# Kernel tuning notes

Hardware: AMD Instinct MI355X
Metric: run time of the kernel (lower is better)

## Reference

```python
import jax, jax.numpy as jnp
import numpy as np

H = 2048      # hidden_size
K = 1024      # bottleneck_size
R = 3         # number of roles
B = 8         # batch
S = 2048      # sequence length
LN_EPS = 1e-5


def setup_inputs() -> dict:
    key = jax.random.key(0)
    ks = jax.random.split(key, 8)
    # torch nn.Linear default init ~ U(-1/sqrt(fan_in), 1/sqrt(fan_in)); scale similarly
    sd_d = 1.0 / np.sqrt(H)
    sd_u = 1.0 / np.sqrt(K)
    return {
        "role": jax.random.randint(ks[0], (B,), 0, R),
        "hidden_states": jax.random.normal(ks[1], (B, S, H), dtype=jnp.float32),
        # stacked per-role adapter params
        "W_down": jax.random.uniform(ks[2], (R, H, K), jnp.float32, -sd_d, sd_d),
        "b_down": jax.random.uniform(ks[3], (R, K), jnp.float32, -sd_d, sd_d),
        "W_up": jax.random.uniform(ks[4], (R, K, H), jnp.float32, -sd_u, sd_u),
        "b_up": jax.random.uniform(ks[5], (R, H), jnp.float32, -sd_u, sd_u),
        "gamma": jnp.ones((R, H), jnp.float32),
        "beta": jnp.zeros((R, H), jnp.float32),
    }


def reference(role, hidden_states, W_down, b_down, W_up, b_up, gamma, beta):
    # gather per-sample adapter params by role id: [B, H, K] etc.
    h = jnp.einsum("bsh,bhk->bsk", hidden_states, W_down[role]) + b_down[role][:, None, :]
    h = jax.nn.gelu(h, approximate=False)  # torch nn.GELU default = exact erf
    u = jnp.einsum("bsk,bkh->bsh", h, W_up[role]) + b_up[role][:, None, :]
    y = hidden_states + u
    # LayerNorm over last dim
    mean = jnp.mean(y, axis=-1, keepdims=True)
    var = jnp.mean(jnp.square(y - mean), axis=-1, keepdims=True)
    yn = (y - mean) * jax.lax.rsqrt(var + LN_EPS)
    return yn * gamma[role][:, None, :] + beta[role][:, None, :]
```

## Files before the change

kernel.cpp:

```cpp
#include <hip/hip_runtime.h>
#include <hip/hip_bf16.h>

#define H 2048
#define K 1024
#define R 3
#define BB 8
#define S 2048

typedef __bf16 bf16x8 __attribute__((ext_vector_type(8)));
typedef float f32x4 __attribute__((ext_vector_type(4)));
typedef unsigned short ushort8 __attribute__((ext_vector_type(8)));

static __device__ __forceinline__ unsigned short f2bf(float f) {
    unsigned int u = __float_as_uint(f);
    u += 0x7FFFu + ((u >> 16) & 1u);
    return (unsigned short)(u >> 16);
}

#define GLOAD_LDS16(g, l)                                                      \
    __builtin_amdgcn_global_load_lds(                                          \
        (const __attribute__((address_space(1))) void*)(g),                    \
        (__attribute__((address_space(3))) void*)(l), 16, 0, 0)

__global__ __launch_bounds__(256) void cvt_hs(const float* __restrict__ in,
                                              unsigned short* __restrict__ out,
                                              int n8) {
    int stride = gridDim.x * blockDim.x;
    for (int i = blockIdx.x * blockDim.x + threadIdx.x; i < n8; i += stride) {
        const float4* p = (const float4*)(in + (size_t)i * 8);
        float4 a = p[0], b = p[1];
        union { unsigned short us[8]; ushort8 v; } o;
        o.us[0] = f2bf(a.x); o.us[1] = f2bf(a.y);
        o.us[2] = f2bf(a.z); o.us[3] = f2bf(a.w);
        o.us[4] = f2bf(b.x); o.us[5] = f2bf(b.y);
        o.us[6] = f2bf(b.z); o.us[7] = f2bf(b.w);
        *(ushort8*)(out + (size_t)i * 8) = o.v;
    }
}

__global__ __launch_bounds__(256) void tpose(const float* __restrict__ in,
                                             unsigned short* __restrict__ out,
                                             int rows, int cols) {
    __shared__ float tile[32][33];
    int rr = blockIdx.z;
    const float* ip = in + (size_t)rr * rows * cols;
    unsigned short* op = out + (size_t)rr * rows * cols;
    int x = blockIdx.x * 32 + threadIdx.x;
    int y0 = blockIdx.y * 32 + threadIdx.y;
#pragma unroll
    for (int j = 0; j < 32; j += 8)
        tile[threadIdx.y + j][threadIdx.x] = ip[(size_t)(y0 + j) * cols + x];
    __syncthreads();
    int ox = blockIdx.y * 32 + threadIdx.x;
    int oy0 = blockIdx.x * 32 + threadIdx.y;
#pragma unroll
    for (int j = 0; j < 32; j += 8)
        op[(size_t)(oy0 + j) * rows + ox] = f2bf(tile[threadIdx.x][threadIdx.y + j]);
}

template <int KC, int EPI>
__global__ __launch_bounds__(512, 2) void gemm_8ph(
    const unsigned short* __restrict__ A, const unsigned short* __restrict__ Bt,
    const int* __restrict__ role, const float* __restrict__ bias,
    const unsigned short* __restrict__ resid, void* __restrict__ Out,
    float2* __restrict__ Part, int N) {
    constexpr int NT = KC / 64;
    __shared__ char smem[131072];
    const int tid = threadIdx.x;
    const int wid = tid >> 6, lane = tid & 63;
    const int wm = wid >> 2, wn = wid & 3;
    const int lr = lane & 15, lc = lane >> 4;

    const int nx = N >> 8;
    const int cpx = gridDim.x >> 3;
    const int orig = (blockIdx.x & 7) * cpx + (blockIdx.x >> 3);
    const int tn = orig % nx;
    const int tmz = orig / nx;
    const int tm = tmz & 7;
    const int z = tmz >> 3;
    const int r = role[z];

    const char* Ab = (const char*)(A + ((size_t)z * S + (size_t)tm * 256) * KC);
    const char* Bb = (const char*)(Bt + ((size_t)r * N + (size_t)tn * 256) * KC);

    const int P16 = tid * 16;

#define STAGE16(gbase, ldsoff, kt, half)                                       \
    do {                                                                       \
        _Pragma("unroll") for (int c_ = 0; c_ < 2; c_++) {                     \
            int P_ = c_ * 8192 + P16;                                          \
            int L_ = P_ ^ (((P_ >> 7) & 7) << 4);                              \
            const char* g_ = (gbase) +                                         \
                (size_t)((half) * 128 + (L_ >> 7)) * (KC * 2) +                \
                (size_t)(kt) * 128 + (L_ & 127);                               \
            GLOAD_LDS16(g_, smem + (ldsoff) + (half) * 16384 + P_);            \
        }                                                                      \
    } while (0)

    STAGE16(Ab, 0, 0, 0);        STAGE16(Ab, 0, 0, 1);
    STAGE16(Bb, 32768, 0, 0);    STAGE16(Bb, 32768, 0, 1);
    STAGE16(Bb, 98304, 1, 0);    STAGE16(Bb, 98304, 1, 1);
    asm volatile("s_waitcnt vmcnt(4)" ::: "memory");
    __builtin_amdgcn_s_barrier();

    f32x4 acc[8][4] = {};
    const int swz = (lr & 7) << 4;
    const int ck0 = (lc << 4) ^ swz;
    const int ck1 = ck0 ^ 0x40;
    const char* sm = smem;

#define LDA4(ibase, SL)                                                        \
    _Pragma("unroll") for (int i_ = 0; i_ < 4; i_++) {                         \
        int rb_ = (wm * 128 + ((ibase) + i_) * 16 + lr) << 7;                  \
        a[i_][0] = *(const bf16x8*)(sm + (SL) + rb_ + ck0);                    \
        a[i_][1] = *(const bf16x8*)(sm + (SL) + rb_ + ck1); }
#define LDB2(jbase, SL)                                                        \
    _Pragma("unroll") for (int j_ = 0; j_ < 2; j_++) {                         \
        int rb_ = (wn * 64 + ((jbase) + j_) * 16 + lr) << 7;                   \
        b[(jbase) + j_][0] = *(const bf16x8*)(sm + (SL) + 32768 + rb_ + ck0);  \
        b[(jbase) + j_][1] = *(const bf16x8*)(sm + (SL) + 32768 + rb_ + ck1); }
#define MFMA16(IOFF, JOFF)                                                     \
    _Pragma("unroll") for (int kk = 0; kk < 2; kk++)                           \
    _Pragma("unroll") for (int i_ = 0; i_ < 4; i_++)                           \
    _Pragma("unroll") for (int j_ = 0; j_ < 2; j_++)                           \
        acc[(IOFF) + i_][(JOFF) + j_] = __builtin_amdgcn_mfma_f32_16x16x32_bf16( \
            a[i_][kk], b[(JOFF) + j_][kk], acc[(IOFF) + i_][(JOFF) + j_], 0, 0, 0);
#define PH_MID()                                                               \
    __builtin_amdgcn_s_barrier();                                              \
    asm volatile("s_waitcnt lgkmcnt(0)" ::: "memory");                         \
    __builtin_amdgcn_s_setprio(1);
#define PH_END()                                                               \
    __builtin_amdgcn_s_setprio(0);                                             \
    __builtin_amdgcn_s_barrier();

#pragma unroll 1
    for (int t = 0; t < NT; t += 2) {
        bf16x8 a[4][2], b[4][2];
        const bool pf2 = (t + 2) < NT, pf3 = (t + 3) < NT;
        LDA4(0, 0); LDB2(0, 0);
        STAGE16(Ab, 65536, t + 1, 0);
        asm volatile("s_waitcnt lgkmcnt(8)" ::: "memory");
        PH_MID(); MFMA16(0, 0); PH_END();
        LDB2(2, 0);
        STAGE16(Ab, 65536, t + 1, 1);
        PH_MID(); MFMA16(0, 2); PH_END();
        LDA4(4, 0);
        if (pf2) STAGE16(Bb, 32768, t + 2, 0);
        PH_MID(); MFMA16(4, 0); PH_END();
        if (pf2) STAGE16(Bb, 32768, t + 2, 1);
        PH_MID(); MFMA16(4, 2);
        __builtin_amdgcn_s_setprio(0);
        if (pf2) asm volatile("s_waitcnt vmcnt(4)" ::: "memory");
        else     asm volatile("s_waitcnt vmcnt(0)" ::: "memory");
        __builtin_amdgcn_s_barrier();
        LDA4(0, 65536); LDB2(0, 65536);
        if (pf2) STAGE16(Ab, 0, t + 2, 0);
        asm volatile("s_waitcnt lgkmcnt(8)" ::: "memory");
        PH_MID(); MFMA16(0, 0); PH_END();
        LDB2(2, 65536);
        if (pf2) STAGE16(Ab, 0, t + 2, 1);
        PH_MID(); MFMA16(0, 2); PH_END();
        LDA4(4, 65536);
        if (pf3) STAGE16(Bb, 98304, t + 3, 0);
        PH_MID(); MFMA16(4, 0); PH_END();
        if (pf3) STAGE16(Bb, 98304, t + 3, 1);
        PH_MID(); MFMA16(4, 2);
        __builtin_amdgcn_s_setprio(0);
        if (pf2) {
            if (pf3) asm volatile("s_waitcnt vmcnt(4)" ::: "memory");
            else     asm volatile("s_waitcnt vmcnt(0)" ::: "memory");
            __builtin_amdgcn_s_barrier();
        }
    }
#undef STAGE16
#undef LDA4
#undef LDB2
#undef MFMA16
#undef PH_MID
#undef PH_END

    const int base_m = tm * 256 + wm * 128;
    const int base_n = tn * 256 + wn * 64;
    float bn[4];
    const float* bp = bias + (size_t)r * N + base_n;
#pragma unroll
    for (int j = 0; j < 4; j++) bn[j] = bp[j * 16 + lr];

    if (EPI == 0) {
        unsigned short* o = (unsigned short*)Out;
#pragma unroll
        for (int i = 0; i < 8; i++) {
#pragma unroll
            for (int j = 0; j < 4; j++) {
#pragma unroll
                for (int q = 0; q < 4; q++) {
                    size_t grow = (size_t)z * S + base_m + i * 16 + lc * 4 + q;
                    int col = base_n + j * 16 + lr;
                    float x = acc[i][j][q] + bn[j];
                    float g = 0.5f * x * (1.0f + erff(x * 0.70710678118654752f));
                    o[grow * N + col] = f2bf(g);
                }
            }
        }
    } else {
        unsigned short* o = (unsigned short*)Out;
        float* pl = (float*)smem;
        __syncthreads();
#pragma unroll
        for (int i = 0; i < 8; i++) {
#pragma unroll
            for (int q = 0; q < 4; q++) {
                size_t grow = (size_t)z * S + base_m + i * 16 + lc * 4 + q;
                float s = 0.f, sq = 0.f;
#pragma unroll
                for (int j = 0; j < 4; j++) {
                    int col = base_n + j * 16 + lr;
                    float rv = __uint_as_float(((unsigned)resid[grow * (size_t)N + col]) << 16);
                    float y = acc[i][j][q] + bn[j] + rv;
                    o[grow * (size_t)N + col] = f2bf(y);
                    s += y; sq += y * y;
                }
#pragma unroll
                for (int off = 1; off < 16; off <<= 1) {
                    s  += __shfl_xor(s, off);
                    sq += __shfl_xor(sq, off);
                }
                if (lr == 0) {
                    int rloc = wm * 128 + i * 16 + lc * 4 + q;
                    pl[wn * 256 + rloc] = s;
                    pl[(4 + wn) * 256 + rloc] = sq;
                }
            }
        }
        __syncthreads();
        if (tid < 256) {
            float s  = pl[tid] + pl[256 + tid] + pl[512 + tid] + pl[768 + tid];
            float sq = pl[1024 + tid] + pl[1280 + tid] + pl[1536 + tid] + pl[1792 + tid];
            size_t grow = (size_t)z * S + tm * 256 + tid;
            Part[(size_t)tn * (BB * S) + grow] = make_float2(s, sq);
        }
    }
}

__global__ __launch_bounds__(256) void ln2(const unsigned short* __restrict__ ybf,
                                           const float2* __restrict__ part,
                                           const int* __restrict__ role,
                                           const float* __restrict__ gamma,
                                           const float* __restrict__ beta,
                                           float* __restrict__ out) {
    int row = blockIdx.x;
    int z = row >> 11;
    int r = role[z];
    float s = 0.f, ss = 0.f;
#pragma unroll
    for (int nb = 0; nb < 8; nb++) {
        float2 p = part[(size_t)nb * (BB * S) + row];
        s += p.x; ss += p.y;
    }
    float mean = s * (1.0f / H);
    float var = ss * (1.0f / H) - mean * mean;
    float rstd = rsqrtf(var + 1e-5f);
    int t = threadIdx.x;
    ushort8 yv = ((const ushort8*)(ybf + (size_t)row * H))[t];
    const float4* gp = (const float4*)(gamma + (size_t)r * H);
    const float4* bp = (const float4*)(beta + (size_t)r * H);
    float4 g0 = gp[2 * t], g1 = gp[2 * t + 1];
    float4 b0 = bp[2 * t], b1 = bp[2 * t + 1];
    float yo[8];
#pragma unroll
    for (int e = 0; e < 8; e++)
        yo[e] = (__uint_as_float(((unsigned)yv[e]) << 16) - mean) * rstd;
    float4 r0, r1;
    r0.x = yo[0] * g0.x + b0.x; r0.y = yo[1] * g0.y + b0.y;
    r0.z = yo[2] * g0.z + b0.z; r0.w = yo[3] * g0.w + b0.w;
    r1.x = yo[4] * g1.x + b1.x; r1.y = yo[5] * g1.y + b1.y;
    r1.z = yo[6] * g1.z + b1.z; r1.w = yo[7] * g1.w + b1.w;
    float4* op = (float4*)(out + (size_t)row * H);
    op[2 * t] = r0;
    op[2 * t + 1] = r1;
}

extern "C" void kernel_launch(void* const* d_in, const int* in_sizes, int n_in,
                              void* d_out, int out_size, void* d_ws, size_t ws_size,
                              hipStream_t stream) {
    const int* role = (const int*)d_in[0];
    const float* hs = (const float*)d_in[1];
    const float* Wd = (const float*)d_in[2];
    const float* bd = (const float*)d_in[3];
    const float* Wu = (const float*)d_in[4];
    const float* bu = (const float*)d_in[5];
    const float* gamma = (const float*)d_in[6];
    const float* beta = (const float*)d_in[7];
    float* out = (float*)d_out;

    char* ws = (char*)d_ws;
    unsigned short* hs_bf = (unsigned short*)ws;
    unsigned short* y_bf = (unsigned short*)ws;
    unsigned short* wd_t = (unsigned short*)(ws + 67108864);
    float2* part = (float2*)(ws + 67108864);
    unsigned short* wu_t = (unsigned short*)(ws + 67108864 + 12582912);
    unsigned short* h_ws = (unsigned short*)(ws + 67108864 + 2 * 12582912);

    cvt_hs<<<4096, 256, 0, stream>>>(hs, hs_bf, (BB * S * H) / 8);
    dim3 tb(32, 8);
    tpose<<<dim3(K / 32, H / 32, R), tb, 0, stream>>>(Wd, wd_t, H, K);
    tpose<<<dim3(H / 32, K / 32, R), tb, 0, stream>>>(Wu, wu_t, K, H);
    gemm_8ph<H, 0><<<(K / 256) * 8 * BB, 512, 0, stream>>>(hs_bf, wd_t, role, bd,
                                                           nullptr, h_ws, nullptr, K);
    gemm_8ph<K, 1><<<(H / 256) * 8 * BB, 512, 0, stream>>>(h_ws, wu_t, role, bu,
                                                           hs_bf, y_bf, part, H);
    ln2<<<BB * S, 256, 0, stream>>>(y_bf, part, role, gamma, beta, out);
}
```

Baseline: 256.0 us.

## Software-pipeline LDS fragment reads one phase ahead of MFMA in GEMM loop

Restructures the GEMM main loop so LDS fragment reads for the next quadrant are issued before the MFMAs of the current quadrant. A and B fragments are double-buffered in registers (aA/aB, bL/bH), and the per-phase barrier/lgkmcnt(0) pairs are replaced with a single barrier per phase. The first tile's fragments are read in a prologue. The intent is to hide LDS latency behind matrix work and cut barrier count. This costs more VGPRs, and the relaxed vmcnt and barrier placement risks races on the staged buffers.

```diff
diff --git a/kernel.cpp b/kernel.cpp
--- a/kernel.cpp
+++ b/kernel.cpp
@@ -101,7 +101,7 @@
     STAGE16(Bb, 32768, 0, 0);    STAGE16(Bb, 32768, 0, 1);
     STAGE16(Bb, 98304, 1, 0);    STAGE16(Bb, 98304, 1, 1);
     asm volatile("s_waitcnt vmcnt(4)" ::: "memory");
-    __builtin_amdgcn_s_barrier();
+    asm volatile("s_barrier" ::: "memory");
 
     f32x4 acc[8][4] = {};
     const int swz = (lr & 7) << 4;
@@ -109,75 +109,75 @@
     const int ck1 = ck0 ^ 0x40;
     const char* sm = smem;
 
-#define LDA4(ibase, SL)                                                        \
+    bf16x8 aA[4][2], aB[4][2], bL[2][2], bH[2][2];
+
+#define RDA(dst, ibase, SL)                                                    \
     _Pragma("unroll") for (int i_ = 0; i_ < 4; i_++) {                         \
         int rb_ = (wm * 128 + ((ibase) + i_) * 16 + lr) << 7;                  \
-        a[i_][0] = *(const bf16x8*)(sm + (SL) + rb_ + ck0);                    \
-        a[i_][1] = *(const bf16x8*)(sm + (SL) + rb_ + ck1); }
-#define LDB2(jbase, SL)                                                        \
+        dst[i_][0] = *(const bf16x8*)(sm + (SL) + rb_ + ck0);                  \
+        dst[i_][1] = *(const bf16x8*)(sm + (SL) + rb_ + ck1); }
+#define RDB(dst, jbase, SL)                                                    \
     _Pragma("unroll") for (int j_ = 0; j_ < 2; j_++) {                         \
         int rb_ = (wn * 64 + ((jbase) + j_) * 16 + lr) << 7;                   \
-        b[(jbase) + j_][0] = *(const bf16x8*)(sm + (SL) + 32768 + rb_ + ck0);  \
-        b[(jbase) + j_][1] = *(const bf16x8*)(sm + (SL) + 32768 + rb_ + ck1); }
-#define MFMA16(IOFF, JOFF)                                                     \
+        dst[j_][0] = *(const bf16x8*)(sm + (SL) + 32768 + rb_ + ck0);          \
+        dst[j_][1] = *(const bf16x8*)(sm + (SL) + 32768 + rb_ + ck1); }
+#define QMFMA(ar, br, IOFF, JOFF)                                              \
     _Pragma("unroll") for (int kk = 0; kk < 2; kk++)                           \
     _Pragma("unroll") for (int i_ = 0; i_ < 4; i_++)                           \
     _Pragma("unroll") for (int j_ = 0; j_ < 2; j_++)                           \
         acc[(IOFF) + i_][(JOFF) + j_] = __builtin_amdgcn_mfma_f32_16x16x32_bf16( \
-            a[i_][kk], b[(JOFF) + j_][kk], acc[(IOFF) + i_][(JOFF) + j_], 0, 0, 0);
-#define PH_MID()                                                               \
-    __builtin_amdgcn_s_barrier();                                              \
-    asm volatile("s_waitcnt lgkmcnt(0)" ::: "memory");                         \
-    __builtin_amdgcn_s_setprio(1);
-#define PH_END()                                                               \
-    __builtin_amdgcn_s_setprio(0);                                             \
-    __builtin_amdgcn_s_barrier();
+            ar[i_][kk], br[j_][kk], acc[(IOFF) + i_][(JOFF) + j_], 0, 0, 0);
+#define BAR() asm volatile("s_barrier" ::: "memory")
+
+    RDA(aA, 0, 0);
+    RDB(bL, 0, 0);
 
 #pragma unroll 1
     for (int t = 0; t < NT; t += 2) {
-        bf16x8 a[4][2], b[4][2];
-        const bool pf2 = (t + 2) < NT, pf3 = (t + 3) < NT;
-        LDA4(0, 0); LDB2(0, 0);
+        const bool pf = (t + 2) < NT;
+        RDB(bH, 2, 0);
         STAGE16(Ab, 65536, t + 1, 0);
-        asm volatile("s_waitcnt lgkmcnt(8)" ::: "memory");
-        PH_MID(); MFMA16(0, 0); PH_END();
-        LDB2(2, 0);
+        __builtin_amdgcn_s_setprio(1); QMFMA(aA, bL, 0, 0);
+        __builtin_amdgcn_s_setprio(0); BAR();
+        RDA(aB, 4, 0);
         STAGE16(Ab, 65536, t + 1, 1);
-        PH_MID(); MFMA16(0, 2); PH_END();
-        LDA4(4, 0);
-        if (pf2) STAGE16(Bb, 32768, t + 2, 0);
-        PH_MID(); MFMA16(4, 0); PH_END();
-        if (pf2) STAGE16(Bb, 32768, t + 2, 1);
-        PH_MID(); MFMA16(4, 2);
+        __builtin_amdgcn_s_setprio(1); QMFMA(aA, bH, 0, 2);
+        __builtin_amdgcn_s_setprio(0); BAR();
+        if (pf) STAGE16(Bb, 32768, t + 2, 0);
+        __builtin_amdgcn_s_setprio(1); QMFMA(aB, bL, 4, 0);
         __builtin_amdgcn_s_setprio(0);
-        if (pf2) asm volatile("s_waitcnt vmcnt(4)" ::: "memory");
-        else     asm volatile("s_waitcnt vmcnt(0)" ::: "memory");
-        __builtin_amdgcn_s_barrier();
-        LDA4(0, 65536); LDB2(0, 65536);
-        if (pf2) STAGE16(Ab, 0, t + 2, 0);
-        asm volatile("s_waitcnt lgkmcnt(8)" ::: "memory");
-        PH_MID(); MFMA16(0, 0); PH_END();
-        LDB2(2, 65536);
-        if (pf2) STAGE16(Ab, 0, t + 2, 1);
-        PH_MID(); MFMA16(0, 2); PH_END();
-        LDA4(4, 65536);
-        if (pf3) STAGE16(Bb, 98304, t + 3, 0);
-        PH_MID(); MFMA16(4, 0); PH_END();
-        if (pf3) STAGE16(Bb, 98304, t + 3, 1);
-        PH_MID(); MFMA16(4, 2);
+        if (pf) asm volatile("s_waitcnt vmcnt(2)" ::: "memory");
+        else    asm volatile("s_waitcnt vmcnt(0)" ::: "memory");
+        BAR();
+        RDA(aA, 0, 65536);
+        RDB(bL, 0, 65536);
+        if (pf) STAGE16(Bb, 32768, t + 2, 1);
+        __builtin_amdgcn_s_setprio(1); QMFMA(aB, bH, 4, 2);
+        __builtin_amdgcn_s_setprio(0); BAR();
+        RDB(bH, 2, 65536);
+        if (pf) STAGE16(Ab, 0, t + 2, 0);
+        __builtin_amdgcn_s_setprio(1); QMFMA(aA, bL, 0, 0);
+        __builtin_amdgcn_s_setprio(0); BAR();
+        RDA(aB, 4, 65536);
+        if (pf) STAGE16(Ab, 0, t + 2, 1);
+        __builtin_amdgcn_s_setprio(1); QMFMA(aA, bH, 0, 2);
+        __builtin_amdgcn_s_setprio(0); BAR();
+        if (pf) STAGE16(Bb, 98304, t + 3, 0);
+        __builtin_amdgcn_s_setprio(1); QMFMA(aB, bL, 4, 0);
         __builtin_amdgcn_s_setprio(0);
-        if (pf2) {
-            if (pf3) asm volatile("s_waitcnt vmcnt(4)" ::: "memory");
-            else     asm volatile("s_waitcnt vmcnt(0)" ::: "memory");
-            __builtin_amdgcn_s_barrier();
-        }
+        if (pf) asm volatile("s_waitcnt vmcnt(2)" ::: "memory");
+        BAR();
+        if (pf) { RDA(aA, 0, 0); RDB(bL, 0, 0); }
+        if (pf) STAGE16(Bb, 98304, t + 3, 1);
+        __builtin_amdgcn_s_setprio(1); QMFMA(aB, bH, 4, 2);
+        __builtin_amdgcn_s_setprio(0);
+        if (pf) BAR();
     }
 #undef STAGE16
-#undef LDA4
-#undef LDB2
-#undef MFMA16
-#undef PH_MID
-#undef PH_END
+#undef RDA
+#undef RDB
+#undef QMFMA
+#undef BAR
 
     const int base_m = tm * 256 + wm * 128;
     const int base_n = tn * 256 + wn * 64;
```

New measurement: 315.2 us. 23.1% more time.

## Replace 8-phase GEMM with smaller-tile triple-buffered kernel for higher occupancy

Applied to the files above, without the earlier changes.

Swaps the hand-scheduled 8-phase 256x256 GEMM for a 128x256 tile with a K-step of 32, triple-buffered LDS staging, and a simpler single-barrier loop. LDS per block drops to 72KB and launch bounds allow 4 blocks per CU, so the kernel relies on thread-level parallelism rather than intra-wave phase interleaving to hide latency. This doubles the grid size and B-tile reloads per output and adds more barriers per unit of work. It may also lose the fine-grained MFMA/load overlap of the previous schedule.

```diff
diff --git a/kernel.cpp b/kernel.cpp
--- a/kernel.cpp
+++ b/kernel.cpp
@@ -59,13 +59,13 @@
 }
 
 template <int KC, int EPI>
-__global__ __launch_bounds__(512, 2) void gemm_8ph(
+__global__ __launch_bounds__(512, 4) void gemm_tlp(
     const unsigned short* __restrict__ A, const unsigned short* __restrict__ Bt,
     const int* __restrict__ role, const float* __restrict__ bias,
     const unsigned short* __restrict__ resid, void* __restrict__ Out,
     float2* __restrict__ Part, int N) {
-    constexpr int NT = KC / 64;
-    __shared__ char smem[131072];
+    constexpr int NT = KC / 32;
+    __shared__ char smem[73728];
     const int tid = threadIdx.x;
     const int wid = tid >> 6, lane = tid & 63;
     const int wm = wid >> 2, wn = wid & 3;
@@ -76,110 +76,65 @@
     const int orig = (blockIdx.x & 7) * cpx + (blockIdx.x >> 3);
     const int tn = orig % nx;
     const int tmz = orig / nx;
-    const int tm = tmz & 7;
-    const int z = tmz >> 3;
+    const int tm = tmz & 15;
+    const int z = tmz >> 4;
     const int r = role[z];
 
-    const char* Ab = (const char*)(A + ((size_t)z * S + (size_t)tm * 256) * KC);
+    const char* Ab = (const char*)(A + ((size_t)z * S + (size_t)tm * 128) * KC);
     const char* Bb = (const char*)(Bt + ((size_t)r * N + (size_t)tn * 256) * KC);
 
     const int P16 = tid * 16;
-
-#define STAGE16(gbase, ldsoff, kt, half)                                       \
-    do {                                                                       \
-        _Pragma("unroll") for (int c_ = 0; c_ < 2; c_++) {                     \
-            int P_ = c_ * 8192 + P16;                                          \
-            int L_ = P_ ^ (((P_ >> 7) & 7) << 4);                              \
-            const char* g_ = (gbase) +                                         \
-                (size_t)((half) * 128 + (L_ >> 7)) * (KC * 2) +                \
-                (size_t)(kt) * 128 + (L_ & 127);                               \
-            GLOAD_LDS16(g_, smem + (ldsoff) + (half) * 16384 + P_);            \
-        }                                                                      \
-    } while (0)
-
-    STAGE16(Ab, 0, 0, 0);        STAGE16(Ab, 0, 0, 1);
-    STAGE16(Bb, 32768, 0, 0);    STAGE16(Bb, 32768, 0, 1);
-    STAGE16(Bb, 98304, 1, 0);    STAGE16(Bb, 98304, 1, 1);
-    asm volatile("s_waitcnt vmcnt(4)" ::: "memory");
+    const int srowA = P16 >> 6;
+    const int sslot = ((P16 >> 4) & 3) ^ ((srowA >> 1) & 3);
+    const size_t sgA = (size_t)srowA * (KC * 2) + sslot * 16;
+
+#define STGA(sb, kt) GLOAD_LDS16(Ab + sgA + (kt) * 64, smem + (sb) + P16)
+#define STGB(sb, kt, c)                                                        \
+    GLOAD_LDS16(Bb + (size_t)((c) * 128 + srowA) * (KC * 2) + sslot * 16 +     \
+                    (kt) * 64,                                                 \
+                smem + (sb) + 8192 + (c) * 8192 + P16)
+#define STAGE3(sb, kt) do { STGA(sb, kt); STGB(sb, kt, 0); STGB(sb, kt, 1); } while (0)
+
+    STAGE3(0, 0);
+    STAGE3(24576, 1);
+    asm volatile("s_waitcnt vmcnt(3)" ::: "memory");
     __builtin_amdgcn_s_barrier();
 
-    f32x4 acc[8][4] = {};
-    const int swz = (lr & 7) << 4;
-    const int ck0 = (lc << 4) ^ swz;
-    const int ck1 = ck0 ^ 0x40;
+    f32x4 acc[4][4] = {};
+    const int ck = (lc ^ ((lr >> 1) & 3)) << 4;
     const char* sm = smem;
 
-#define LDA4(ibase, SL)                                                        \
-    _Pragma("unroll") for (int i_ = 0; i_ < 4; i_++) {                         \
-        int rb_ = (wm * 128 + ((ibase) + i_) * 16 + lr) << 7;                  \
-        a[i_][0] = *(const bf16x8*)(sm + (SL) + rb_ + ck0);                    \
-        a[i_][1] = *(const bf16x8*)(sm + (SL) + rb_ + ck1); }
-#define LDB2(jbase, SL)                                                        \
-    _Pragma("unroll") for (int j_ = 0; j_ < 2; j_++) {                         \
-        int rb_ = (wn * 64 + ((jbase) + j_) * 16 + lr) << 7;                   \
-        b[(jbase) + j_][0] = *(const bf16x8*)(sm + (SL) + 32768 + rb_ + ck0);  \
-        b[(jbase) + j_][1] = *(const bf16x8*)(sm + (SL) + 32768 + rb_ + ck1); }
-#define MFMA16(IOFF, JOFF)                                                     \
-    _Pragma("unroll") for (int kk = 0; kk < 2; kk++)                           \
-    _Pragma("unroll") for (int i_ = 0; i_ < 4; i_++)                           \
-    _Pragma("unroll") for (int j_ = 0; j_ < 2; j_++)                           \
-        acc[(IOFF) + i_][(JOFF) + j_] = __builtin_amdgcn_mfma_f32_16x16x32_bf16( \
-            a[i_][kk], b[(JOFF) + j_][kk], acc[(IOFF) + i_][(JOFF) + j_], 0, 0, 0);
-#define PH_MID()                                                               \
-    __builtin_amdgcn_s_barrier();                                              \
-    asm volatile("s_waitcnt lgkmcnt(0)" ::: "memory");                         \
-    __builtin_amdgcn_s_setprio(1);
-#define PH_END()                                                               \
-    __builtin_amdgcn_s_setprio(0);                                             \
-    __builtin_amdgcn_s_barrier();
-
+    int sA = 0, sB = 24576, sC = 49152;
 #pragma unroll 1
-    for (int t = 0; t < NT; t += 2) {
-        bf16x8 a[4][2], b[4][2];
-        const bool pf2 = (t + 2) < NT, pf3 = (t + 3) < NT;
-        LDA4(0, 0); LDB2(0, 0);
-        STAGE16(Ab, 65536, t + 1, 0);
-        asm volatile("s_waitcnt lgkmcnt(8)" ::: "memory");
-        PH_MID(); MFMA16(0, 0); PH_END();
-        LDB2(2, 0);
-        STAGE16(Ab, 65536, t + 1, 1);
-        PH_MID(); MFMA16(0, 2); PH_END();
-        LDA4(4, 0);
-        if (pf2) STAGE16(Bb, 32768, t + 2, 0);
-        PH_MID(); MFMA16(4, 0); PH_END();
-        if (pf2) STAGE16(Bb, 32768, t + 2, 1);
-        PH_MID(); MFMA16(4, 2);
+    for (int t = 0; t < NT; ++t) {
+        const bool pf = (t + 2) < NT;
+        if (pf) STAGE3(sC, t + 2);
+        bf16x8 a[4], b[4];
+#pragma unroll
+        for (int i = 0; i < 4; i++)
+            a[i] = *(const bf16x8*)(sm + sA + ((wm * 64 + i * 16 + lr) << 6) + ck);
+#pragma unroll
+        for (int j = 0; j < 4; j++)
+            b[j] = *(const bf16x8*)(sm + sA + 8192 + ((wn * 64 + j * 16 + lr) << 6) + ck);
+        __builtin_amdgcn_s_setprio(1);
+#pragma unroll
+        for (int i = 0; i < 4; i++)
+#pragma unroll
+            for (int j = 0; j < 4; j++)
+                acc[i][j] = __builtin_amdgcn_mfma_f32_16x16x32_bf16(a[i], b[j], acc[i][j], 0, 0, 0);
         __builtin_amdgcn_s_setprio(0);
-        if (pf2) asm volatile("s_waitcnt vmcnt(4)" ::: "memory");
-        else     asm volatile("s_waitcnt vmcnt(0)" ::: "memory");
-        __builtin_amdgcn_s_barrier();
-        LDA4(0, 65536); LDB2(0, 65536);
-        if (pf2) STAGE16(Ab, 0, t + 2, 0);
-        asm volatile("s_waitcnt lgkmcnt(8)" ::: "memory");
-        PH_MID(); MFMA16(0, 0); PH_END();
-        LDB2(2, 65536);
-        if (pf2) STAGE16(Ab, 0, t + 2, 1);
-        PH_MID(); MFMA16(0, 2); PH_END();
-        LDA4(4, 65536);
-        if (pf3) STAGE16(Bb, 98304, t + 3, 0);
-        PH_MID(); MFMA16(4, 0); PH_END();
-        if (pf3) STAGE16(Bb, 98304, t + 3, 1);
-        PH_MID(); MFMA16(4, 2);
-        __builtin_amdgcn_s_setprio(0);
-        if (pf2) {
-            if (pf3) asm volatile("s_waitcnt vmcnt(4)" ::: "memory");
-            else     asm volatile("s_waitcnt vmcnt(0)" ::: "memory");
+        if (t < NT - 1) {
+            if (pf) asm volatile("s_waitcnt vmcnt(3)" ::: "memory");
+            else    asm volatile("s_waitcnt vmcnt(0)" ::: "memory");
             __builtin_amdgcn_s_barrier();
         }
-    }
-#undef STAGE16
-#undef LDA4
-#undef LDB2
-#undef MFMA16
-#undef PH_MID
-#undef PH_END
-
-    const int base_m = tm * 256 + wm * 128;
+        int tmp = sA; sA = sB; sB = sC; sC = tmp;
+    }
+#undef STGA
+#undef STGB
+#undef STAGE3
+
+    const int base_m = tm * 128 + wm * 64;
     const int base_n = tn * 256 + wn * 64;
     float bn[4];
     const float* bp = bias + (size_t)r * N + base_n;
@@ -189,7 +144,7 @@
     if (EPI == 0) {
         unsigned short* o = (unsigned short*)Out;
 #pragma unroll
-        for (int i = 0; i < 8; i++) {
+        for (int i = 0; i < 4; i++) {
 #pragma unroll
             for (int j = 0; j < 4; j++) {
 #pragma unroll
@@ -207,7 +162,7 @@
         float* pl = (float*)smem;
         __syncthreads();
 #pragma unroll
-        for (int i = 0; i < 8; i++) {
+        for (int i = 0; i < 4; i++) {
 #pragma unroll
             for (int q = 0; q < 4; q++) {
                 size_t grow = (size_t)z * S + base_m + i * 16 + lc * 4 + q;
@@ -226,17 +181,17 @@
                     sq += __shfl_xor(sq, off);
                 }
                 if (lr == 0) {
-                    int rloc = wm * 128 + i * 16 + lc * 4 + q;
-                    pl[wn * 256 + rloc] = s;
-                    pl[(4 + wn) * 256 + rloc] = sq;
+                    int rloc = wm * 64 + i * 16 + lc * 4 + q;
+                    pl[wn * 128 + rloc] = s;
+                    pl[512 + wn * 128 + rloc] = sq;
                 }
             }
         }
         __syncthreads();
-        if (tid < 256) {
-            float s  = pl[tid] + pl[256 + tid] + pl[512 + tid] + pl[768 + tid];
-            float sq = pl[1024 + tid] + pl[1280 + tid] + pl[1536 + tid] + pl[1792 + tid];
-            size_t grow = (size_t)z * S + tm * 256 + tid;
+        if (tid < 128) {
+            float s  = pl[tid] + pl[128 + tid] + pl[256 + tid] + pl[384 + tid];
+            float sq = pl[512 + tid] + pl[640 + tid] + pl[768 + tid] + pl[896 + tid];
+            size_t grow = (size_t)z * S + tm * 128 + tid;
             Part[(size_t)tn * (BB * S) + grow] = make_float2(s, sq);
         }
     }
@@ -305,9 +260,9 @@
     dim3 tb(32, 8);
     tpose<<<dim3(K / 32, H / 32, R), tb, 0, stream>>>(Wd, wd_t, H, K);
     tpose<<<dim3(H / 32, K / 32, R), tb, 0, stream>>>(Wu, wu_t, K, H);
-    gemm_8ph<H, 0><<<(K / 256) * 8 * BB, 512, 0, stream>>>(hs_bf, wd_t, role, bd,
-                                                           nullptr, h_ws, nullptr, K);
-    gemm_8ph<K, 1><<<(H / 256) * 8 * BB, 512, 0, stream>>>(h_ws, wu_t, role, bu,
-                                                           hs_bf, y_bf, part, H);
+    gemm_tlp<H, 0><<<(K / 256) * 16 * BB, 512, 0, stream>>>(hs_bf, wd_t, role, bd,
+                                                            nullptr, h_ws, nullptr, K);
+    gemm_tlp<K, 1><<<(H / 256) * 16 * BB, 512, 0, stream>>>(h_ws, wu_t, role, bu,
+                                                            hs_bf, y_bf, part, H);
     ln2<<<BB * S, 256, 0, stream>>>(y_bf, part, role, gamma, beta, out);
 }
```

Result: no change. 259.7 us, median of 2 (+1.5%).
